# Kernel tuning notes

Hardware: AMD Instinct MI355X
Metric: run time of the kernel (lower is better)

The kernel has to match this reference:

```python
import jax, jax.numpy as jnp
import numpy as np

B, S, D, H = 4, 2048, 512, 8
INNER = D  # assumed AttentionHead.inner_size == size (naive single-head attention)


def setup_inputs() -> dict:
    key = jax.random.key(0)
    ks = jax.random.split(key, 8)
    scale = 0.02
    return {
        "emb_input": jax.random.normal(ks[0], (B, S, D), dtype=jnp.float32),
        "Wq": jax.random.normal(ks[1], (H, D, INNER), dtype=jnp.float32) * scale,
        "bq": jnp.zeros((H, INNER), dtype=jnp.float32),
        "Wk": jax.random.normal(ks[2], (H, D, INNER), dtype=jnp.float32) * scale,
        "bk": jnp.zeros((H, INNER), dtype=jnp.float32),
        "Wv": jax.random.normal(ks[3], (H, D, INNER), dtype=jnp.float32) * scale,
        "bv": jnp.zeros((H, INNER), dtype=jnp.float32),
        "Wp": jax.random.normal(ks[4], (H * INNER, D), dtype=jnp.float32) * scale,
        "bp": jnp.zeros((D,), dtype=jnp.float32),
    }


def reference(emb_input, Wq, bq, Wk, bk, Wv, bv, Wp, bp):
    # All heads batched into one einsum instead of a Python loop over submodules.
    x = emb_input  # [B, S, D]
    q = jnp.einsum("bsd,hde->bhse", x, Wq) + bq[None, :, None, :]  # [B,H,S,E]
    k = jnp.einsum("bsd,hde->bhse", x, Wk) + bk[None, :, None, :]
    v = jnp.einsum("bsd,hde->bhse", x, Wv) + bv[None, :, None, :]
    scores = jnp.einsum("bhse,bhte->bhst", q, k) / jnp.sqrt(
        jnp.asarray(INNER, dtype=x.dtype)
    )  # [B,H,S,S]
    attn = jax.nn.softmax(scores, axis=-1)
    o = jnp.einsum("bhst,bhte->bhse", attn, v)  # [B,H,S,E]
    # concat over heads (dim=2 in torch => feature dim after per-head outputs)
    o = jnp.transpose(o, (0, 2, 1, 3)).reshape(B, S, H * INNER)
    return o @ Wp + bp  # [B, S, D]
```

## Files before the change

kernel.cpp:

```cpp
#include <hip/hip_runtime.h>


typedef short s8v __attribute__((ext_vector_type(8)));
typedef float f4v __attribute__((ext_vector_type(4)));
typedef unsigned short us;
typedef us us4v __attribute__((ext_vector_type(4)));

__device__ inline us f2b(float f) {
  union { float f; unsigned u; } v; v.f = f;
  unsigned r = v.u + 0x7FFFu + ((v.u >> 16) & 1u);
  return (us)(r >> 16);
}

__device__ inline void gld16(const us* g, us* l) {
  __builtin_amdgcn_global_load_lds(
      (const __attribute__((address_space(1))) void*)g,
      (__attribute__((address_space(3))) void*)l, 16, 0, 0);
}

template <int EPI>
__global__ __launch_bounds__(512, 4) void gemm_nt(
    const us* __restrict__ A, int lda, long long sA0, long long sA1,
    const us* __restrict__ Bm, int ldb, long long sB0, long long sB1,
    const float* __restrict__ bias, const float* __restrict__ bias2,
    const float* __restrict__ bias3,
    void* __restrict__ Cv, void* __restrict__ C2, void* __restrict__ C3,
    int ldc, long long sC0, long long sC1,
    int K, float alpha, int L, int sbits) {
  __shared__ us As[2][8192];
  __shared__ us Bs[2][4096];
  const int t = threadIdx.x;
  const int wv = t >> 6, ln = t & 63;
  const int m16 = ln & 15, quad = ln >> 4;

  const int gx = gridDim.x, gxy = gx * gridDim.y;
  const int nblk = gxy * gridDim.z;
  const int flat = blockIdx.x + gx * blockIdx.y + gxy * blockIdx.z;
  int nid = flat;
  if ((nblk & 7) == 0) nid = (flat & 7) * (nblk >> 3) + (flat >> 3);
  const int bz = nid / gxy, rem = nid % gxy;
  const int by = rem / gx, bx = rem % gx;

  const long long row0 = (long long)by * 256;
  const long long col0 = (long long)bx * 128;
  const int zo = bz >> L, zi = bz & ((1 << L) - 1);
  const us* Az = A + zo * sA0 + zi * sA1;
  const us* Bz = Bm + zo * sB0 + zi * sB1;

  int offA[2], offB;
#pragma unroll
  for (int j = 0; j < 2; ++j) {
    const int c = t + 512 * j;
    const int mb = c >> 6, qd = (c >> 4) & 3, mm = c & 15;
    offA[j] = (int)((row0 + mb * 16 + mm) * (long long)lda + qd * 8);
  }
  {
    const int mb = t >> 6, qd = (t >> 4) & 3, mm = t & 15;
    offB = (int)((col0 + mb * 16 + mm) * (long long)ldb + qd * 8);
  }

  f4v acc[4][4];
#pragma unroll
  for (int r = 0; r < 4; ++r)
#pragma unroll
    for (int c = 0; c < 4; ++c) acc[r][c] = (f4v){0.f, 0.f, 0.f, 0.f};

  const int nk = K >> 5;
  const int fo = quad * 16 + m16;
  const int arow = wv & 3, bcol = wv >> 2;

#pragma unroll
  for (int j = 0; j < 2; ++j)
    gld16(Az + offA[j], (us*)As[0] + (512 * j + wv * 64) * 8);
  gld16(Bz + offB, (us*)Bs[0] + (wv * 64) * 8);

  for (int i = 0; i < nk; ++i) {
    __syncthreads();
    const int cur = i & 1;
    if (i + 1 < nk) {
      const int kof = (i + 1) << 5;
#pragma unroll
      for (int j = 0; j < 2; ++j)
        gld16(Az + offA[j] + kof, (us*)As[cur ^ 1] + (512 * j + wv * 64) * 8);
      gld16(Bz + offB + kof, (us*)Bs[cur ^ 1] + (wv * 64) * 8);
    }
    s8v af[4], bf[4];
#pragma unroll
    for (int r = 0; r < 4; ++r)
      af[r] = *(const s8v*)&As[cur][((arow * 4 + r) * 64 + fo) * 8];
#pragma unroll
    for (int c = 0; c < 4; ++c)
      bf[c] = *(const s8v*)&Bs[cur][((bcol * 4 + c) * 64 + fo) * 8];
#pragma unroll
    for (int r = 0; r < 4; ++r)
#pragma unroll
      for (int c = 0; c < 4; ++c)
        acc[r][c] = __builtin_amdgcn_mfma_f32_16x16x32_bf16(af[r], bf[c], acc[r][c], 0, 0, 0);
  }

  if (EPI == 6) {
#pragma unroll
    for (int r = 0; r < 4; ++r)
#pragma unroll
      for (int c = 0; c < 4; ++c)
#pragma unroll
        for (int g = 0; g < 4; ++g)
          acc[r][c][g] = __expf(fmaf(acc[r][c][g], alpha, -4.f));
  }
#pragma unroll
  for (int r = 0; r < 4; ++r) {
    const int inRow = arow * 64 + r * 16 + quad * 4;
    const long long gr0 = row0 + inRow;
#pragma unroll
    for (int c = 0; c < 4; ++c) {
      const long long gc = col0 + bcol * 64 + c * 16 + m16;
      if (EPI == 3) {
        const int which = (int)(gc >> sbits);
        const int gsec = (int)gc & ((1 << sbits) - 1);
        const int hc = gsec >> 9, e = (int)gc & 511;
        const long long slice =
            ((long long)zo * (1 << (sbits - 9)) + hc) * 1048576LL;
        if (which == 0) {
          us* C = (us*)Cv;
          const float bb = bias[gsec];
#pragma unroll
          for (int g = 0; g < 4; ++g)
            C[slice + (gr0 + g) * 512 + e] = f2b(acc[r][c][g] + bb);
        } else if (which == 1) {
          us* C = (us*)C2;
          const float bb = bias2[gsec];
#pragma unroll
          for (int g = 0; g < 4; ++g)
            C[slice + (gr0 + g) * 512 + e] = f2b(acc[r][c][g] + bb);
        } else {
          us* C = (us*)C3;
          const float bb = bias3[gsec];
          us4v pk;
#pragma unroll
          for (int g = 0; g < 4; ++g) pk[g] = f2b(acc[r][c][g] + bb);
          *(us4v*)&C[slice + (long long)e * 2048 + gr0] = pk;
        }
      } else if (EPI == 5) {
        float* C = (float*)Cv + zo * sC0;
        float* p = C + gr0 * ldc + gc;
#pragma unroll
        for (int g = 0; g < 4; ++g)
          atomicAdd(&p[(long long)g * ldc], acc[r][c][g] * alpha);
      } else if (EPI == 6) {
        us* C = (us*)Cv + zo * sC0 + zi * sC1;
#pragma unroll
        for (int g = 0; g < 4; ++g)
          C[(gr0 + g) * (long long)ldc + gc] = f2b(acc[r][c][g]);
      } else {
        us* C = (us*)Cv + zo * sC0 + zi * sC1;
        const float* lrow = (const float*)C2 + (long long)bz * 2048;
#pragma unroll
        for (int g = 0; g < 4; ++g) {
          const float inv = 1.f / lrow[gr0 + g];
          C[(gr0 + g) * (long long)ldc + gc] = f2b(acc[r][c][g] * inv);
        }
      }
    }
    if (EPI == 6) {
      float* lsum = (float*)C2 + (long long)bz * 2048;
#pragma unroll
      for (int g = 0; g < 4; ++g) {
        float s = acc[r][0][g] + acc[r][1][g] + acc[r][2][g] + acc[r][3][g];
        s += __shfl_xor(s, 1, 64);
        s += __shfl_xor(s, 2, 64);
        s += __shfl_xor(s, 4, 64);
        s += __shfl_xor(s, 8, 64);
        if (m16 == 0) atomicAdd(&lsum[gr0 + g], s);
      }
    }
  }
}

__global__ __launch_bounds__(256) void conv_bf16(const float* __restrict__ in,
                                                 us* __restrict__ out, int n4) {
  const int i = blockIdx.x * 256 + threadIdx.x;
  if (i < n4) {
    const float4 f = ((const float4*)in)[i];
    us4v o;
    o[0] = f2b(f.x); o[1] = f2b(f.y); o[2] = f2b(f.z); o[3] = f2b(f.w);
    ((us4v*)out)[i] = o;
  }
}

__global__ __launch_bounds__(256) void conv_transpose(const float* __restrict__ in,
                                                      us* __restrict__ out,
                                                      int R, int C, int Lc,
                                                      int mask, long long sChunk) {
  __shared__ float tile[32][33];
  const int tx = threadIdx.x & 31, ty = threadIdx.x >> 5;
  const int z = blockIdx.z;
  const long long zi = (long long)z * R * C;
  us* dst = out + (long long)(z >> Lc) * sChunk + (long long)(z & mask) * R * C;
  const int r0 = blockIdx.y * 32, c0 = blockIdx.x * 32;
#pragma unroll
  for (int j = 0; j < 4; ++j)
    tile[ty + 8 * j][tx] = in[zi + (long long)(r0 + ty + 8 * j) * C + c0 + tx];
  __syncthreads();
#pragma unroll
  for (int j = 0; j < 4; ++j)
    dst[(long long)(c0 + ty + 8 * j) * R + r0 + tx] = f2b(tile[tx][ty + 8 * j]);
}

__global__ __launch_bounds__(256) void init_out_kernel(float* __restrict__ out,
                                                       const float* __restrict__ bp,
                                                       int total,
                                                       float* __restrict__ lz,
                                                       int lcnt) {
  const int i = blockIdx.x * 256 + threadIdx.x;
  if (i < total) out[i] = bp[i & 511];
  else if (i < total + lcnt) lz[i - total] = 0.f;
}

extern "C" void kernel_launch(void* const* d_in, const int* in_sizes, int n_in,
                              void* d_out, int out_size, void* d_ws, size_t ws_size,
                              hipStream_t stream) {
  constexpr int Bb = 4, S = 2048, D = 512, H = 8, E = 512, HE = 4096;
  const float* x  = (const float*)d_in[0];
  const float* Wq = (const float*)d_in[1];
  const float* bq = (const float*)d_in[2];
  const float* Wk = (const float*)d_in[3];
  const float* bk = (const float*)d_in[4];
  const float* Wv = (const float*)d_in[5];
  const float* bv = (const float*)d_in[6];
  const float* Wp = (const float*)d_in[7];
  const float* bp = (const float*)d_in[8];
  float* out = (float*)d_out;

  const long long SE = (long long)S * E, SS = (long long)S * S;
  const long long SD = (long long)S * D, ED = (long long)E * D;

  us* xh  = (us*)d_ws;
  us* W3  = xh + 4194304;
  us* WpT = W3 + 6291456;
  us* dyn = WpT + 2097152;

  const size_t fixedB = (size_t)(4194304 + 6291456 + 2097152) * 2;
  const size_t lB = (size_t)H * Bb * S * 4;
  int HC = 8;
  while (HC > 1) {
    const size_t need = fixedB + lB +
        (size_t)HC * (3 * (size_t)Bb * SE + (size_t)Bb * SS) * 2;
    if (need <= ws_size) break;
    HC >>= 1;
  }
  const int Lh = (HC == 8) ? 3 : (HC == 4) ? 2 : (HC == 2) ? 1 : 0;
  const int BHC = Bb * HC;
  const int sbits = 9 + Lh;

  us* qh = dyn;
  us* kh = qh + (size_t)BHC * SE;
  us* vT = kh + (size_t)BHC * SE;
  us* sc = vT + (size_t)BHC * SE;
  float* lb = (float*)(sc + (size_t)BHC * SS);
  us* oh = qh;

  const dim3 tb(256), tg(512);
  const int lcnt = H * Bb * S;
  init_out_kernel<<<dim3((Bb * S * D + lcnt + 255) / 256), tb, 0, stream>>>(
      out, bp, Bb * S * D, lb, lcnt);
  conv_bf16<<<dim3(4194304 / 4 / 256), tb, 0, stream>>>(x, xh, 4194304 / 4);
  const long long sChunk = 3LL * HC * ED;
  conv_transpose<<<dim3(16, 16, H), tb, 0, stream>>>(Wq, W3, D, E, Lh, HC - 1, sChunk);
  conv_transpose<<<dim3(16, 16, H), tb, 0, stream>>>(Wk, W3 + HC * ED, D, E, Lh, HC - 1, sChunk);
  conv_transpose<<<dim3(16, 16, H), tb, 0, stream>>>(Wv, W3 + 2 * HC * ED, D, E, Lh, HC - 1, sChunk);
  conv_transpose<<<dim3(16, 128, 1), tb, 0, stream>>>(Wp, WpT, HE, D, 0, 0, 0);

  const float aS = 0.044194173824159216f;
  const dim3 gQKV(3 * HC * E / 128, 8, Bb);
  const dim3 gS(16, 8, BHC);
  const dim3 gPV(4, 8, BHC);
  const dim3 gOP(4, 8, BHC);

  for (int c = 0; c < H / HC; ++c) {
    const int h0 = c * HC;
    float* lc = lb + (long long)c * BHC * S;
    gemm_nt<3><<<gQKV, tg, 0, stream>>>(
        xh, D, SD, 0, W3 + c * sChunk, D, 0, 0,
        bq + h0 * E, bk + h0 * E, bv + h0 * E,
        qh, kh, vT, 512, 0, SE, D, 1.f, 0, sbits);
    gemm_nt<6><<<gS, tg, 0, stream>>>(
        qh, E, (long long)HC * SE, SE, kh, E, (long long)HC * SE, SE,
        nullptr, nullptr, nullptr, sc, lc, nullptr,
        S, (long long)HC * SS, SS, E, aS, Lh, 0);
    gemm_nt<7><<<gPV, tg, 0, stream>>>(
        sc, S, (long long)HC * SS, SS, vT, S, (long long)HC * SE, SE,
        nullptr, nullptr, nullptr, oh, lc, nullptr,
        HC * E, (long long)S * HC * E, E, S, 1.f, Lh, 0);
    gemm_nt<5><<<gOP, tg, 0, stream>>>(
        oh, HC * E, (long long)S * HC * E, 512,
        WpT + (long long)h0 * E, HE, 0, 512,
        nullptr, nullptr, nullptr, out, nullptr, nullptr,
        D, SD, 0, 512, 1.f, Lh, 0);
  }
}
```

Before: 949.9 us.

## Enlarge GEMM tile to 256x256 with K=64 stages and ping-pong scheduling

The bf16 MFMA GEMM now uses a 256x256 output tile per block instead of 256x128, and each K step covers 64 elements. Both A and B tiles are double-buffered and prefetched two stages ahead, with waits on the vector-memory counter. Within a step, waves barrier between LDS loads and MFMA bursts under raised priority. The goal is more data reuse per LDS byte and better overlap of loads with matrix math. The cost is twice the accumulator registers, about 128KB of LDS, and lower occupancy (launch bound 2). Grids are halved in the column dimension to match.

Result: slower. 1.046 ms (+10.1%).

```diff
diff --git a/kernel.cpp b/kernel.cpp
--- a/kernel.cpp
+++ b/kernel.cpp
@@ -19,7 +19,7 @@
 }
 
 template <int EPI>
-__global__ __launch_bounds__(512, 4) void gemm_nt(
+__global__ __launch_bounds__(512, 2) void gemm_nt(
     const us* __restrict__ A, int lda, long long sA0, long long sA1,
     const us* __restrict__ Bm, int ldb, long long sB0, long long sB1,
     const float* __restrict__ bias, const float* __restrict__ bias2,
@@ -27,8 +27,8 @@
     void* __restrict__ Cv, void* __restrict__ C2, void* __restrict__ C3,
     int ldc, long long sC0, long long sC1,
     int K, float alpha, int L, int sbits) {
-  __shared__ us As[2][8192];
-  __shared__ us Bs[2][4096];
+  __shared__ __align__(16) us As[2][16384];
+  __shared__ __align__(16) us Bs[2][16384];
   const int t = threadIdx.x;
   const int wv = t >> 6, ln = t & 63;
   const int m16 = ln & 15, quad = ln >> 4;
@@ -42,65 +42,89 @@
   const int by = rem / gx, bx = rem % gx;
 
   const long long row0 = (long long)by * 256;
-  const long long col0 = (long long)bx * 128;
+  const long long col0 = (long long)bx * 256;
   const int zo = bz >> L, zi = bz & ((1 << L) - 1);
   const us* Az = A + zo * sA0 + zi * sA1;
   const us* Bz = Bm + zo * sB0 + zi * sB1;
 
-  int offA[2], offB;
-#pragma unroll
-  for (int j = 0; j < 2; ++j) {
+  int offA[4], offB[4];
+#pragma unroll
+  for (int j = 0; j < 4; ++j) {
     const int c = t + 512 * j;
-    const int mb = c >> 6, qd = (c >> 4) & 3, mm = c & 15;
-    offA[j] = (int)((row0 + mb * 16 + mm) * (long long)lda + qd * 8);
-  }
-  {
-    const int mb = t >> 6, qd = (t >> 4) & 3, mm = t & 15;
-    offB = (int)((col0 + mb * 16 + mm) * (long long)ldb + qd * 8);
-  }
-
-  f4v acc[4][4];
-#pragma unroll
-  for (int r = 0; r < 4; ++r)
+    const int s = c >> 6, l = c & 63;
+    const int mb = s >> 1, ks = s & 1, qd = (l >> 4) & 3, mm = l & 15;
+    offA[j] = (int)((row0 + mb * 16 + mm) * (long long)lda + ks * 32 + qd * 8);
+    offB[j] = (int)((col0 + mb * 16 + mm) * (long long)ldb + ks * 32 + qd * 8);
+  }
+
+  f4v acc[8][4];
+#pragma unroll
+  for (int r = 0; r < 8; ++r)
 #pragma unroll
     for (int c = 0; c < 4; ++c) acc[r][c] = (f4v){0.f, 0.f, 0.f, 0.f};
 
-  const int nk = K >> 5;
-  const int fo = quad * 16 + m16;
-  const int arow = wv & 3, bcol = wv >> 2;
-
-#pragma unroll
-  for (int j = 0; j < 2; ++j)
-    gld16(Az + offA[j], (us*)As[0] + (512 * j + wv * 64) * 8);
-  gld16(Bz + offB, (us*)Bs[0] + (wv * 64) * 8);
-
-  for (int i = 0; i < nk; ++i) {
-    __syncthreads();
-    const int cur = i & 1;
-    if (i + 1 < nk) {
-      const int kof = (i + 1) << 5;
-#pragma unroll
-      for (int j = 0; j < 2; ++j)
-        gld16(Az + offA[j] + kof, (us*)As[cur ^ 1] + (512 * j + wv * 64) * 8);
-      gld16(Bz + offB + kof, (us*)Bs[cur ^ 1] + (wv * 64) * 8);
+  const int nk = K >> 6;
+  const int wr = wv >> 2, wc = wv & 3;
+
+#define STAGE(kt2, bb)                                                        \
+  {                                                                           \
+    const int kof = (kt2) << 6;                                               \
+    _Pragma("unroll") for (int j = 0; j < 4; ++j)                             \
+        gld16(Az + offA[j] + kof, (us*)As[bb] + (t + 512 * j) * 8);           \
+    _Pragma("unroll") for (int j = 0; j < 4; ++j)                             \
+        gld16(Bz + offB[j] + kof, (us*)Bs[bb] + (t + 512 * j) * 8);           \
+  }
+
+  STAGE(0, 0);
+  STAGE(1, 1);
+
+  for (int kt = 0; kt < nk; ++kt) {
+    const int b = kt & 1;
+    if (kt + 1 < nk)
+      asm volatile("s_waitcnt vmcnt(8)" ::: "memory");
+    else
+      asm volatile("s_waitcnt vmcnt(0)" ::: "memory");
+    __builtin_amdgcn_s_barrier();
+
+    s8v bfr[8];
+#pragma unroll
+    for (int c = 0; c < 4; ++c)
+#pragma unroll
+      for (int ks = 0; ks < 2; ++ks)
+        bfr[c * 2 + ks] =
+            *(const s8v*)&Bs[b][(((wc * 4 + c) * 2 + ks) * 64 + ln) * 8];
+
+#pragma unroll
+    for (int p = 0; p < 4; ++p) {
+      s8v af[4];
+#pragma unroll
+      for (int rr = 0; rr < 2; ++rr)
+#pragma unroll
+        for (int ks = 0; ks < 2; ++ks)
+          af[rr * 2 + ks] = *(const s8v*)&As[b]
+              [(((wr * 8 + p * 2 + rr) * 2 + ks) * 64 + ln) * 8];
+      __builtin_amdgcn_s_barrier();
+      asm volatile("s_waitcnt lgkmcnt(0)" ::: "memory");
+      __builtin_amdgcn_sched_barrier(0);
+      __builtin_amdgcn_s_setprio(1);
+#pragma unroll
+      for (int ks = 0; ks < 2; ++ks)
+#pragma unroll
+        for (int rr = 0; rr < 2; ++rr)
+#pragma unroll
+          for (int c = 0; c < 4; ++c)
+            acc[p * 2 + rr][c] = __builtin_amdgcn_mfma_f32_16x16x32_bf16(
+                af[rr * 2 + ks], bfr[c * 2 + ks], acc[p * 2 + rr][c], 0, 0, 0);
+      __builtin_amdgcn_s_setprio(0);
+      __builtin_amdgcn_s_barrier();
     }
-    s8v af[4], bf[4];
-#pragma unroll
-    for (int r = 0; r < 4; ++r)
-      af[r] = *(const s8v*)&As[cur][((arow * 4 + r) * 64 + fo) * 8];
-#pragma unroll
-    for (int c = 0; c < 4; ++c)
-      bf[c] = *(const s8v*)&Bs[cur][((bcol * 4 + c) * 64 + fo) * 8];
-#pragma unroll
-    for (int r = 0; r < 4; ++r)
-#pragma unroll
-      for (int c = 0; c < 4; ++c)
-        acc[r][c] = __builtin_amdgcn_mfma_f32_16x16x32_bf16(af[r], bf[c], acc[r][c], 0, 0, 0);
-  }
+    if (kt + 2 < nk) STAGE(kt + 2, b);
+  }
+#undef STAGE
 
   if (EPI == 6) {
 #pragma unroll
-    for (int r = 0; r < 4; ++r)
+    for (int r = 0; r < 8; ++r)
 #pragma unroll
       for (int c = 0; c < 4; ++c)
 #pragma unroll
@@ -108,12 +132,12 @@
           acc[r][c][g] = __expf(fmaf(acc[r][c][g], alpha, -4.f));
   }
 #pragma unroll
-  for (int r = 0; r < 4; ++r) {
-    const int inRow = arow * 64 + r * 16 + quad * 4;
+  for (int r = 0; r < 8; ++r) {
+    const int inRow = wr * 128 + r * 16 + quad * 4;
     const long long gr0 = row0 + inRow;
 #pragma unroll
     for (int c = 0; c < 4; ++c) {
-      const long long gc = col0 + bcol * 64 + c * 16 + m16;
+      const long long gc = col0 + wc * 64 + c * 16 + m16;
       if (EPI == 3) {
         const int which = (int)(gc >> sbits);
         const int gsec = (int)gc & ((1 << sbits) - 1);
@@ -271,10 +295,10 @@
   conv_transpose<<<dim3(16, 128, 1), tb, 0, stream>>>(Wp, WpT, HE, D, 0, 0, 0);
 
   const float aS = 0.044194173824159216f;
-  const dim3 gQKV(3 * HC * E / 128, 8, Bb);
-  const dim3 gS(16, 8, BHC);
-  const dim3 gPV(4, 8, BHC);
-  const dim3 gOP(4, 8, BHC);
+  const dim3 gQKV(3 * HC * E / 256, 8, Bb);
+  const dim3 gS(8, 8, BHC);
+  const dim3 gPV(2, 8, BHC);
+  const dim3 gOP(2, 8, BHC);
 
   for (int c = 0; c < H / HC; ++c) {
     const int h0 = c * HC;
```
